# Performance work log

Hardware: AMD Instinct MI355X
Metric: run time of the kernel (lower is better)

The kernel has to match this reference:

```python
import jax, jax.numpy as jnp
import numpy as np

N_NODES = 100000
N_EDGES = 1_600_000
N_ROIS = 400
HIDDEN = 128
N_GRAPHS = 512
OUT = 2


def setup_inputs() -> dict:
    key = jax.random.key(0)
    ks = jax.random.split(key, 7)
    x = jax.random.normal(ks[0], (N_NODES, N_ROIS), dtype=jnp.float32)
    edge_index = jax.random.randint(ks[1], (2, N_EDGES), 0, N_NODES, dtype=jnp.int32)
    # sorted graph-assignment vector; prepend arange so every graph id is non-empty
    rnd = jax.random.randint(ks[2], (N_NODES - N_GRAPHS,), 0, N_GRAPHS, dtype=jnp.int32)
    batch = jnp.sort(jnp.concatenate([jnp.arange(N_GRAPHS, dtype=jnp.int32), rnd]))
    W = jax.random.normal(ks[3], (N_ROIS, HIDDEN), dtype=jnp.float32) / np.float32(np.sqrt(N_ROIS))
    b = jnp.zeros((HIDDEN,), dtype=jnp.float32)
    lin_W = jax.random.normal(ks[4], (HIDDEN, OUT), dtype=jnp.float32) / np.float32(np.sqrt(HIDDEN))
    lin_b = jnp.zeros((OUT,), dtype=jnp.float32)
    return {"x": x, "edge_index": edge_index, "batch": batch,
            "W": W, "b": b, "lin_W": lin_W, "lin_b": lin_b}


def reference(x, edge_index, batch, W, b, lin_W, lin_b):
    N = x.shape[0]
    # GCNConv: add self-loops, symmetric normalization D^-1/2 (A+I) D^-1/2
    loops = jnp.arange(N, dtype=edge_index.dtype)
    row = jnp.concatenate([edge_index[0], loops])  # source
    col = jnp.concatenate([edge_index[1], loops])  # target
    deg = jax.ops.segment_sum(jnp.ones_like(col, dtype=x.dtype), col, num_segments=N)
    dinv = jnp.where(deg > 0, jax.lax.rsqrt(deg), 0.0)
    norm = dinv[row] * dinv[col]                   # [E+N]
    h = x @ W                                      # [N, H] transform before propagate
    msg = h[row] * norm[:, None]                   # [E+N, H]
    agg = jax.ops.segment_sum(msg, col, num_segments=N) + b
    act = jax.nn.relu(agg)                         # [N, H]
    # global max pool over graph ids (all segments guaranteed non-empty)
    pooled = jax.ops.segment_max(act, batch, num_segments=N_GRAPHS)  # [G, H]
    logits = pooled @ lin_W + lin_b                # [G, OUT]
    return logits, pooled
```

## Files before the change

kernel.cpp:

```cpp
#include <hip/hip_runtime.h>
#include <hip/hip_bf16.h>

#define N_NODES 100000
#define N_EDGES 1600000
#define N_ROIS  400
#define RKP     416
#define HID     128
#define N_GRAPHS 512
#define NOUT    2
#define NBUCK   391
#define BCAP    8192
#define ECH     4096
#define NPW     16

typedef __attribute__((ext_vector_type(8))) short short8;
typedef __attribute__((ext_vector_type(4))) float f32x4;

static __device__ __forceinline__ unsigned short f2bf(float f) {
  unsigned u = __float_as_uint(f);
  u += 0x7fffu + ((u >> 16) & 1u);
  return (unsigned short)(u >> 16);
}
static __device__ __forceinline__ float blo(unsigned int u) {
  return __uint_as_float(u << 16);
}
static __device__ __forceinline__ float bhi(unsigned int u) {
  return __uint_as_float(u & 0xffff0000u);
}
static __device__ __forceinline__ void gl2lds16(const void* g, void* l) {
  __builtin_amdgcn_global_load_lds(
      (const __attribute__((address_space(1))) unsigned int*)g,
      (__attribute__((address_space(3))) unsigned int*)l, 16, 0, 0);
}

__global__ __launch_bounds__(256) void bucket_k(
    const int* __restrict__ row, const int* __restrict__ col,
    int* __restrict__ bcnt, unsigned int* __restrict__ pairs) {
  __shared__ int hist[NBUCK];
  __shared__ int base[NBUCK];
  int t = threadIdx.x;
  for (int b = t; b < NBUCK; b += 256) hist[b] = 0;
  __syncthreads();
  int e0 = blockIdx.x * ECH;
  unsigned int pk[16];
  int bk[16], rk[16];
#pragma unroll
  for (int i = 0; i < 16; ++i) {
    int e = e0 + t + i * 256;
    if (e < N_EDGES) {
      int r = row[e], c = col[e];
      bk[i] = c >> 8;
      pk[i] = ((unsigned)r << 8) | (unsigned)(c & 255);
      rk[i] = atomicAdd(&hist[bk[i]], 1);
    } else bk[i] = -1;
  }
  __syncthreads();
  for (int b = t; b < NBUCK; b += 256)
    base[b] = (hist[b] > 0) ? atomicAdd(&bcnt[b], hist[b]) : 0;
  __syncthreads();
#pragma unroll
  for (int i = 0; i < 16; ++i)
    if (bk[i] >= 0) {
      int p = base[bk[i]] + rk[i];
      if (p < BCAP) pairs[(size_t)bk[i] * BCAP + p] = pk[i];
    }
}

__global__ __launch_bounds__(256) void csr_build_k(
    const unsigned int* __restrict__ pairs, const int* __restrict__ bcnt,
    int* __restrict__ csr_row, int* __restrict__ offs, int* __restrict__ cnt,
    float* __restrict__ dinv) {
  __shared__ unsigned int ep[BCAP];
  __shared__ int h[256];
  __shared__ int sc[256];
  __shared__ int cur[256];
  int b = blockIdx.x;
  int t = threadIdx.x;
  int m = min(bcnt[b], BCAP);
  size_t base = (size_t)b * BCAP;
  for (int j = t; j < m; j += 256) ep[j] = pairs[base + j];
  h[t] = 0;
  __syncthreads();
  for (int j = t; j < m; j += 256) atomicAdd(&h[ep[j] & 255u], 1);
  __syncthreads();
  int myc = h[t];
  sc[t] = myc;
  __syncthreads();
  for (int off = 1; off < 256; off <<= 1) {
    int v = (t >= off) ? sc[t - off] : 0;
    __syncthreads();
    sc[t] += v;
    __syncthreads();
  }
  int loff = sc[t] - myc;
  cur[t] = loff;
  int node = b * 256 + t;
  if (node < N_NODES) {
    cnt[node] = myc;
    offs[node] = (int)base + loff;
    dinv[node] = rsqrtf((float)(myc + 1));
  }
  __syncthreads();
  for (int j = t; j < m; j += 256) {
    unsigned int e = ep[j];
    int pos = atomicAdd(&cur[e & 255u], 1);
    csr_row[base + pos] = (int)(e >> 8);
  }
}

__global__ void prep_wt_k(const float* __restrict__ W, unsigned short* __restrict__ Wt) {
  int idx = blockIdx.x * blockDim.x + threadIdx.x;
  if (idx < HID * RKP) {
    int n = idx / RKP, k = idx - n * RKP;
    float v = (k < N_ROIS) ? W[k * HID + n] : 0.f;
    Wt[idx] = f2bf(v);
  }
}

__global__ __launch_bounds__(256) void gemm_k(
    const float* __restrict__ x, const unsigned short* __restrict__ Wt,
    const float* __restrict__ dinv, unsigned short* __restrict__ hp) {
  __shared__ __align__(16) unsigned short Bs[2][512 * 8];
  int t = threadIdx.x;
  int lane = t & 63;
  int wv = t >> 6;
  int row0 = blockIdx.x * 64;
  int mrow = lane & 15;
  int kgrp = lane >> 4;

  int n_a = t & 127, kg_a = t >> 7;
  const unsigned short* wsrc0 = Wt + (size_t)n_a * RKP + kg_a * 8;
  const unsigned short* wsrc1 = wsrc0 + 16;
  unsigned short* ldst0 = &Bs[0][(size_t)wv * 64 * 8];
  unsigned short* ldst1 = ldst0 + 256 * 8;

  int grow_r = row0 + wv * 16 + mrow;
  const float* xp = x + (size_t)min(grow_r, N_NODES - 1) * N_ROIS + kgrp * 8;

  f32x4 acc[8];
#pragma unroll
  for (int i = 0; i < 8; ++i) acc[i] = (f32x4){0.f, 0.f, 0.f, 0.f};

  gl2lds16(wsrc0, ldst0);
  gl2lds16(wsrc1, ldst1);
  __syncthreads();

  for (int s = 0; s < 13; ++s) {
    int kk = s * 32;
    short8 af;
    if (kk + kgrp * 8 < N_ROIS) {
      float4 f0 = *(const float4*)(xp + kk);
      float4 f1 = *(const float4*)(xp + kk + 4);
      af[0] = (short)f2bf(f0.x); af[1] = (short)f2bf(f0.y);
      af[2] = (short)f2bf(f0.z); af[3] = (short)f2bf(f0.w);
      af[4] = (short)f2bf(f1.x); af[5] = (short)f2bf(f1.y);
      af[6] = (short)f2bf(f1.z); af[7] = (short)f2bf(f1.w);
    } else {
#pragma unroll
      for (int u = 0; u < 8; ++u) af[u] = 0;
    }
    if (s < 12) {
      int nb = (s + 1) & 1;
      unsigned short* d0 = &Bs[nb][(size_t)wv * 64 * 8];
      gl2lds16(wsrc0 + (kk + 32), d0);
      gl2lds16(wsrc1 + (kk + 32), d0 + 256 * 8);
    }
    const unsigned short* bb = &Bs[s & 1][0];
#pragma unroll
    for (int nt = 0; nt < 8; ++nt) {
      short8 bf = *(const short8*)&bb[(size_t)(kgrp * 128 + nt * 16 + mrow) * 8];
      acc[nt] = __builtin_amdgcn_mfma_f32_16x16x32_bf16(af, bf, acc[nt], 0, 0, 0);
    }
    __syncthreads();
  }

#pragma unroll
  for (int r = 0; r < 4; ++r) {
    int grow = row0 + wv * 16 + kgrp * 4 + r;
    if (grow < N_NODES) {
      float di = dinv[grow];
      unsigned short* op = hp + (size_t)grow * HID + mrow;
#pragma unroll
      for (int nt = 0; nt < 8; ++nt) {
        op[nt * 16] = f2bf(di * acc[nt][r]);
      }
    }
  }
}

__global__ __launch_bounds__(256) void gather_k(
    const unsigned short* __restrict__ hp, const int* __restrict__ csr_row,
    const int* __restrict__ offs, const int* __restrict__ cnt,
    const float* __restrict__ dinv, const int* __restrict__ batch,
    const float* __restrict__ bias, unsigned int* __restrict__ pooled_bits) {
  int wave = (blockIdx.x * blockDim.x + threadIdx.x) >> 6;
  int lane = threadIdx.x & 63;
  int q = lane >> 4;
  int d = lane & 15;
  int n0 = wave * NPW;
  if (n0 >= N_NODES) return;
  int nend = min(n0 + NPW, N_NODES);
  float4 bb0 = *(const float4*)(bias + d * 8);
  float4 bb1 = *(const float4*)(bias + d * 8 + 4);
  float rm[8];
#pragma unroll
  for (int k = 0; k < 8; ++k) rm[k] = 0.f;
  int cur_g = batch[n0];

  for (int i = n0; i < nend; ++i) {
    int start = offs[i];
    int m = cnt[i];
    float a[8];
    if (q == 0) {
      uint4 u = *(const uint4*)(hp + (size_t)i * HID + d * 8);
      a[0] = blo(u.x); a[1] = bhi(u.x); a[2] = blo(u.y); a[3] = bhi(u.y);
      a[4] = blo(u.z); a[5] = bhi(u.z); a[6] = blo(u.w); a[7] = bhi(u.w);
    } else {
#pragma unroll
      for (int k = 0; k < 8; ++k) a[k] = 0.f;
    }
    for (int j = q; j < m; j += 4) {
      int s = csr_row[start + j];
      uint4 u = *(const uint4*)(hp + (size_t)s * HID + d * 8);
      a[0] += blo(u.x); a[1] += bhi(u.x); a[2] += blo(u.y); a[3] += bhi(u.y);
      a[4] += blo(u.z); a[5] += bhi(u.z); a[6] += blo(u.w); a[7] += bhi(u.w);
    }
#pragma unroll
    for (int k = 0; k < 8; ++k) {
      a[k] += __shfl_xor(a[k], 16, 64);
      a[k] += __shfl_xor(a[k], 32, 64);
    }
    float di = dinv[i];
    float p[8];
    p[0] = fmaxf(fmaf(di, a[0], bb0.x), 0.f);
    p[1] = fmaxf(fmaf(di, a[1], bb0.y), 0.f);
    p[2] = fmaxf(fmaf(di, a[2], bb0.z), 0.f);
    p[3] = fmaxf(fmaf(di, a[3], bb0.w), 0.f);
    p[4] = fmaxf(fmaf(di, a[4], bb1.x), 0.f);
    p[5] = fmaxf(fmaf(di, a[5], bb1.y), 0.f);
    p[6] = fmaxf(fmaf(di, a[6], bb1.z), 0.f);
    p[7] = fmaxf(fmaf(di, a[7], bb1.w), 0.f);
    int g = batch[i];
    if (g != cur_g) {
      if (q == 0) {
#pragma unroll
        for (int k = 0; k < 8; ++k)
          atomicMax(&pooled_bits[cur_g * HID + d * 8 + k], __float_as_uint(rm[k]));
      }
#pragma unroll
      for (int k = 0; k < 8; ++k) rm[k] = 0.f;
      cur_g = g;
    }
#pragma unroll
    for (int k = 0; k < 8; ++k) rm[k] = fmaxf(rm[k], p[k]);
  }
  if (q == 0) {
#pragma unroll
    for (int k = 0; k < 8; ++k)
      atomicMax(&pooled_bits[cur_g * HID + d * 8 + k], __float_as_uint(rm[k]));
  }
}

__global__ void logits_k(const float* __restrict__ pooled, const float* __restrict__ lin_W,
                         const float* __restrict__ lin_b, float* __restrict__ out) {
  int t = blockIdx.x * blockDim.x + threadIdx.x;
  if (t < N_GRAPHS * NOUT) {
    int g = t >> 1, o = t & 1;
    float s = lin_b[o];
    const float* pg = pooled + g * HID;
#pragma unroll 8
    for (int k = 0; k < HID; ++k) s = fmaf(pg[k], lin_W[k * NOUT + o], s);
    out[t] = s;
  }
}

extern "C" void kernel_launch(void* const* d_in, const int* in_sizes, int n_in,
                              void* d_out, int out_size, void* d_ws, size_t ws_size,
                              hipStream_t stream) {
  (void)in_sizes; (void)n_in; (void)ws_size;
  const float* x     = (const float*)d_in[0];
  const int*   ei    = (const int*)d_in[1];
  const int*   row   = ei;
  const int*   col   = ei + N_EDGES;
  const int*   batch = (const int*)d_in[2];
  const float* W     = (const float*)d_in[3];
  const float* b     = (const float*)d_in[4];
  const float* lin_W = (const float*)d_in[5];
  const float* lin_b = (const float*)d_in[6];
  float* out = (float*)d_out;

  char* ws = (char*)d_ws;
  int*   bcnt    = (int*)(ws + 0);
  int*   offs    = (int*)(ws + 4096);
  int*   cnt     = (int*)(ws + 404096);
  float* dinv    = (float*)(ws + 804096);
  unsigned short* Wt = (unsigned short*)(ws + 1204096);
  int*   csr_row = (int*)(ws + 1310720);
  unsigned int* pairs = (unsigned int*)(ws + 14123008);
  unsigned short* hp  = (unsigned short*)(ws + 14123008);

  hipMemsetAsync(bcnt, 0, NBUCK * sizeof(int), stream);
  hipMemsetAsync(d_out, 0, (size_t)out_size * sizeof(float), stream);

  bucket_k<<<(N_EDGES + ECH - 1) / ECH, 256, 0, stream>>>(row, col, bcnt, pairs);
  csr_build_k<<<NBUCK, 256, 0, stream>>>(pairs, bcnt, csr_row, offs, cnt, dinv);
  prep_wt_k<<<(HID * RKP + 255) / 256, 256, 0, stream>>>(W, Wt);
  gemm_k<<<(N_NODES + 63) / 64, 256, 0, stream>>>(x, Wt, dinv, hp);
  {
    int waves = (N_NODES + NPW - 1) / NPW;
    int blocks = (waves * 64 + 255) / 256;
    gather_k<<<blocks, 256, 0, stream>>>(
        hp, csr_row, offs, cnt, dinv, batch, b,
        (unsigned int*)(out + N_GRAPHS * NOUT));
  }
  logits_k<<<(N_GRAPHS * NOUT + 255) / 256, 256, 0, stream>>>(
      out + N_GRAPHS * NOUT, lin_W, lin_b, out);
}
```

Measured before the change: 403.2 us.

## Load GEMM weight tiles directly into registers instead of staging through LDS

```diff
diff --git a/kernel.cpp b/kernel.cpp
--- a/kernel.cpp
+++ b/kernel.cpp
@@ -26,11 +26,6 @@
 }
 static __device__ __forceinline__ float bhi(unsigned int u) {
   return __uint_as_float(u & 0xffff0000u);
-}
-static __device__ __forceinline__ void gl2lds16(const void* g, void* l) {
-  __builtin_amdgcn_global_load_lds(
-      (const __attribute__((address_space(1))) unsigned int*)g,
-      (__attribute__((address_space(3))) unsigned int*)l, 16, 0, 0);
 }
 
 __global__ __launch_bounds__(256) void bucket_k(
@@ -120,59 +115,67 @@
 __global__ __launch_bounds__(256) void gemm_k(
     const float* __restrict__ x, const unsigned short* __restrict__ Wt,
     const float* __restrict__ dinv, unsigned short* __restrict__ hp) {
-  __shared__ __align__(16) unsigned short Bs[2][512 * 8];
   int t = threadIdx.x;
   int lane = t & 63;
   int wv = t >> 6;
   int row0 = blockIdx.x * 64;
   int mrow = lane & 15;
   int kgrp = lane >> 4;
-
-  int n_a = t & 127, kg_a = t >> 7;
-  const unsigned short* wsrc0 = Wt + (size_t)n_a * RKP + kg_a * 8;
-  const unsigned short* wsrc1 = wsrc0 + 16;
-  unsigned short* ldst0 = &Bs[0][(size_t)wv * 64 * 8];
-  unsigned short* ldst1 = ldst0 + 256 * 8;
-
   int grow_r = row0 + wv * 16 + mrow;
   const float* xp = x + (size_t)min(grow_r, N_NODES - 1) * N_ROIS + kgrp * 8;
+  const unsigned short* wp = Wt + (size_t)mrow * RKP + kgrp * 8;
+  int klim = N_ROIS - kgrp * 8;
 
   f32x4 acc[8];
 #pragma unroll
   for (int i = 0; i < 8; ++i) acc[i] = (f32x4){0.f, 0.f, 0.f, 0.f};
 
-  gl2lds16(wsrc0, ldst0);
-  gl2lds16(wsrc1, ldst1);
-  __syncthreads();
-
-  for (int s = 0; s < 13; ++s) {
-    int kk = s * 32;
-    short8 af;
-    if (kk + kgrp * 8 < N_ROIS) {
-      float4 f0 = *(const float4*)(xp + kk);
-      float4 f1 = *(const float4*)(xp + kk + 4);
-      af[0] = (short)f2bf(f0.x); af[1] = (short)f2bf(f0.y);
-      af[2] = (short)f2bf(f0.z); af[3] = (short)f2bf(f0.w);
-      af[4] = (short)f2bf(f1.x); af[5] = (short)f2bf(f1.y);
-      af[6] = (short)f2bf(f1.z); af[7] = (short)f2bf(f1.w);
-    } else {
-#pragma unroll
-      for (int u = 0; u < 8; ++u) af[u] = 0;
-    }
-    if (s < 12) {
-      int nb = (s + 1) & 1;
-      unsigned short* d0 = &Bs[nb][(size_t)wv * 64 * 8];
-      gl2lds16(wsrc0 + (kk + 32), d0);
-      gl2lds16(wsrc1 + (kk + 32), d0 + 256 * 8);
-    }
-    const unsigned short* bb = &Bs[s & 1][0];
-#pragma unroll
-    for (int nt = 0; nt < 8; ++nt) {
-      short8 bf = *(const short8*)&bb[(size_t)(kgrp * 128 + nt * 16 + mrow) * 8];
-      acc[nt] = __builtin_amdgcn_mfma_f32_16x16x32_bf16(af, bf, acc[nt], 0, 0, 0);
-    }
-    __syncthreads();
-  }
+#define LOAD_A(dst, s)                                            \
+  do {                                                            \
+    if ((s) * 32 < klim) {                                        \
+      float4 f0 = *(const float4*)(xp + (s) * 32);                \
+      float4 f1 = *(const float4*)(xp + (s) * 32 + 4);            \
+      dst[0] = (short)f2bf(f0.x); dst[1] = (short)f2bf(f0.y);     \
+      dst[2] = (short)f2bf(f0.z); dst[3] = (short)f2bf(f0.w);     \
+      dst[4] = (short)f2bf(f1.x); dst[5] = (short)f2bf(f1.y);     \
+      dst[6] = (short)f2bf(f1.z); dst[7] = (short)f2bf(f1.w);     \
+    } else {                                                      \
+      dst = (short8){0, 0, 0, 0, 0, 0, 0, 0};                     \
+    }                                                             \
+  } while (0)
+
+#define LOAD_B(dst, s)                                                     \
+  do {                                                                     \
+    _Pragma("unroll")                                                      \
+    for (int nt = 0; nt < 8; ++nt)                                         \
+      dst[nt] = *(const short8*)(wp + (size_t)nt * 16 * RKP + (s) * 32);   \
+  } while (0)
+
+#define MFMA_SET(a, bset)                                                  \
+  do {                                                                     \
+    _Pragma("unroll")                                                      \
+    for (int nt = 0; nt < 8; ++nt)                                         \
+      acc[nt] = __builtin_amdgcn_mfma_f32_16x16x32_bf16(a, bset[nt], acc[nt], 0, 0, 0); \
+  } while (0)
+
+  short8 a0, a1, b0[8], b1[8];
+  LOAD_A(a0, 0);
+  LOAD_B(b0, 0);
+#pragma unroll 1
+  for (int s = 0; s + 2 <= 13; s += 2) {
+    LOAD_A(a1, s + 1);
+    LOAD_B(b1, s + 1);
+    MFMA_SET(a0, b0);
+    if (s + 2 < 13) {
+      LOAD_A(a0, s + 2);
+      LOAD_B(b0, s + 2);
+    }
+    MFMA_SET(a1, b1);
+  }
+  MFMA_SET(a0, b0);
+#undef LOAD_A
+#undef LOAD_B
+#undef MFMA_SET
 
 #pragma unroll
   for (int r = 0; r < 4; ++r) {
```

New measurement: 429.8 us. 1.07x slower.

## Stage GEMM A and B tiles through padded LDS with plain loads

Applied to the files above, without the earlier changes.

```diff
diff --git a/kernel.cpp b/kernel.cpp
--- a/kernel.cpp
+++ b/kernel.cpp
@@ -26,11 +26,6 @@
 }
 static __device__ __forceinline__ float bhi(unsigned int u) {
   return __uint_as_float(u & 0xffff0000u);
-}
-static __device__ __forceinline__ void gl2lds16(const void* g, void* l) {
-  __builtin_amdgcn_global_load_lds(
-      (const __attribute__((address_space(1))) unsigned int*)g,
-      (__attribute__((address_space(3))) unsigned int*)l, 16, 0, 0);
 }
 
 __global__ __launch_bounds__(256) void bucket_k(
@@ -120,7 +115,8 @@
 __global__ __launch_bounds__(256) void gemm_k(
     const float* __restrict__ x, const unsigned short* __restrict__ Wt,
     const float* __restrict__ dinv, unsigned short* __restrict__ hp) {
-  __shared__ __align__(16) unsigned short Bs[2][512 * 8];
+  __shared__ __align__(16) short As[64][40];
+  __shared__ __align__(16) short Bs[HID][40];
   int t = threadIdx.x;
   int lane = t & 63;
   int wv = t >> 6;
@@ -128,47 +124,44 @@
   int mrow = lane & 15;
   int kgrp = lane >> 4;
 
-  int n_a = t & 127, kg_a = t >> 7;
-  const unsigned short* wsrc0 = Wt + (size_t)n_a * RKP + kg_a * 8;
-  const unsigned short* wsrc1 = wsrc0 + 16;
-  unsigned short* ldst0 = &Bs[0][(size_t)wv * 64 * 8];
-  unsigned short* ldst1 = ldst0 + 256 * 8;
-
-  int grow_r = row0 + wv * 16 + mrow;
-  const float* xp = x + (size_t)min(grow_r, N_NODES - 1) * N_ROIS + kgrp * 8;
-
   f32x4 acc[8];
 #pragma unroll
   for (int i = 0; i < 8; ++i) acc[i] = (f32x4){0.f, 0.f, 0.f, 0.f};
 
-  gl2lds16(wsrc0, ldst0);
-  gl2lds16(wsrc1, ldst1);
-  __syncthreads();
-
-  for (int s = 0; s < 13; ++s) {
-    int kk = s * 32;
-    short8 af;
-    if (kk + kgrp * 8 < N_ROIS) {
-      float4 f0 = *(const float4*)(xp + kk);
-      float4 f1 = *(const float4*)(xp + kk + 4);
-      af[0] = (short)f2bf(f0.x); af[1] = (short)f2bf(f0.y);
-      af[2] = (short)f2bf(f0.z); af[3] = (short)f2bf(f0.w);
-      af[4] = (short)f2bf(f1.x); af[5] = (short)f2bf(f1.y);
-      af[6] = (short)f2bf(f1.z); af[7] = (short)f2bf(f1.w);
+  int arow = t >> 2;
+  int akofs = (t & 3) * 8;
+  int brow = t >> 1;
+  int bkofs = (t & 1) * 16;
+  int grow_a = row0 + arow;
+  const float* xp = x + (size_t)grow_a * N_ROIS;
+
+  for (int kk = 0; kk < RKP; kk += 32) {
+    short8 a8;
+    if (grow_a < N_NODES && kk + akofs + 8 <= N_ROIS) {
+      float4 f0 = *(const float4*)(xp + kk + akofs);
+      float4 f1 = *(const float4*)(xp + kk + akofs + 4);
+      a8[0] = (short)f2bf(f0.x); a8[1] = (short)f2bf(f0.y);
+      a8[2] = (short)f2bf(f0.z); a8[3] = (short)f2bf(f0.w);
+      a8[4] = (short)f2bf(f1.x); a8[5] = (short)f2bf(f1.y);
+      a8[6] = (short)f2bf(f1.z); a8[7] = (short)f2bf(f1.w);
     } else {
 #pragma unroll
-      for (int u = 0; u < 8; ++u) af[u] = 0;
-    }
-    if (s < 12) {
-      int nb = (s + 1) & 1;
-      unsigned short* d0 = &Bs[nb][(size_t)wv * 64 * 8];
-      gl2lds16(wsrc0 + (kk + 32), d0);
-      gl2lds16(wsrc1 + (kk + 32), d0 + 256 * 8);
-    }
-    const unsigned short* bb = &Bs[s & 1][0];
+      for (int u = 0; u < 8; ++u) {
+        int k = kk + akofs + u;
+        float f = (grow_a < N_NODES && k < N_ROIS) ? xp[k] : 0.f;
+        a8[u] = (short)f2bf(f);
+      }
+    }
+    *(short8*)&As[arow][akofs] = a8;
+    const short8* wp = (const short8*)(Wt + (size_t)brow * RKP + kk + bkofs);
+    *(short8*)&Bs[brow][bkofs] = wp[0];
+    *(short8*)&Bs[brow][bkofs + 8] = wp[1];
+    __syncthreads();
+
+    short8 af = *(const short8*)&As[wv * 16 + mrow][kgrp * 8];
 #pragma unroll
     for (int nt = 0; nt < 8; ++nt) {
-      short8 bf = *(const short8*)&bb[(size_t)(kgrp * 128 + nt * 16 + mrow) * 8];
+      short8 bf = *(const short8*)&Bs[nt * 16 + mrow][kgrp * 8];
       acc[nt] = __builtin_amdgcn_mfma_f32_16x16x32_bf16(af, bf, acc[nt], 0, 0, 0);
     }
     __syncthreads();
```

After: 391.6 us. 2.9% less time.
